# Performance work log

Hardware: AMD Instinct MI355X
Metric: run time of the kernel (lower is better)

Reference implementation:

```python
import jax, jax.numpy as jnp
import numpy as np

EPS = 1e-6
DROP_RATE = 0.25

def setup_inputs() -> dict:
    key = jax.random.key(0)
    k1, k2, k3 = jax.random.split(key, 3)
    B, S, D = 4, 2048, 2048
    inputs = jax.random.normal(k1, (B, S, D), dtype=jnp.float32)
    # keras 'uniform' initializer: U(-0.05, 0.05)
    W_1 = jax.random.uniform(k2, (D, D), dtype=jnp.float32, minval=-0.05, maxval=0.05)
    W_2 = jax.random.uniform(k3, (D, D), dtype=jnp.float32, minval=-0.05, maxval=0.05)
    return {"inputs": inputs, "W_1": W_1, "W_2": W_2}

def reference(inputs, W_1, W_2):
    # LayerNorm over last axis (no affine: gamma/beta unused in original call)
    mean = jnp.mean(inputs, axis=-1, keepdims=True)
    var = jnp.mean(jnp.square(inputs - mean), axis=-1, keepdims=True)
    x_norm = (inputs - mean) / jnp.sqrt(var + EPS)          # [B,S,D]
    # 2-layer MLP with relu
    h = jax.nn.relu(jnp.einsum('bsd,de->bse', x_norm, W_1))  # [B,S,D]
    y = jnp.einsum('bsd,de->bse', h, W_2)                    # [B,S,D]
    # dropout(0.25), inverted scaling, fixed key for determinism
    keep = jax.random.bernoulli(jax.random.key(1), 1.0 - DROP_RATE, y.shape)
    y_drop = jnp.where(keep, y / (1.0 - DROP_RATE), 0.0)
    return x_norm + y_drop
```

## Files before the change

kernel.cpp:

```cpp
#include <hip/hip_runtime.h>
#include <hip/hip_bf16.h>
#include <stdint.h>

#define M_DIM 8192
#define N_DIM 2048
#define K_DIM 2048

typedef __bf16 bf16x8_t __attribute__((ext_vector_type(8)));
typedef float f32x4_t __attribute__((ext_vector_type(4)));
typedef float f32x16_t __attribute__((ext_vector_type(16)));

__device__ __forceinline__ unsigned tf_rotl(unsigned x, int r) {
  return (x << r) | (x >> (32 - r));
}
__device__ __forceinline__ unsigned threefry_mask_bits(unsigned ctr) {
  unsigned x0 = 0u, x1 = ctr;
  const unsigned ks0 = 0u, ks1 = 1u, ks2 = 0x1BD11BDBu;
  x0 += ks0; x1 += ks1;
#define TFR(r) { x0 += x1; x1 = tf_rotl(x1, (r)); x1 ^= x0; }
  TFR(13) TFR(15) TFR(26) TFR(6)
  x0 += ks1; x1 += ks2 + 1u;
  TFR(17) TFR(29) TFR(16) TFR(24)
  x0 += ks2; x1 += ks0 + 2u;
  TFR(13) TFR(15) TFR(26) TFR(6)
  x0 += ks0; x1 += ks1 + 3u;
  TFR(17) TFR(29) TFR(16) TFR(24)
  x0 += ks1; x1 += ks2 + 4u;
  TFR(13) TFR(15) TFR(26) TFR(6)
  x0 += ks2; x1 += ks0 + 5u;
#undef TFR
  return x0 ^ x1;
}

__device__ __forceinline__ void gload_lds16(const __hip_bfloat16* g, unsigned short* l) {
  __builtin_amdgcn_global_load_lds(
      (const __attribute__((address_space(1))) unsigned int*)g,
      (__attribute__((address_space(3))) unsigned int*)l,
      16, 0, 0);
}

__global__ __launch_bounds__(256) void prep_kernel(
    const float* __restrict__ X,  __hip_bfloat16* __restrict__ Xn,
    const float* __restrict__ W1, const float* __restrict__ W2,
    __hip_bfloat16* __restrict__ W1t, __hip_bfloat16* __restrict__ W2t) {
  const int bid = blockIdx.x;
  if (bid < M_DIM) {
    const int row = bid;
    const float4* xv = (const float4*)(X + (size_t)row * K_DIM);
    float4 v0 = xv[threadIdx.x];
    float4 v1 = xv[threadIdx.x + 256];
    float s  = v0.x + v0.y + v0.z + v0.w + v1.x + v1.y + v1.z + v1.w;
    float ss = v0.x*v0.x + v0.y*v0.y + v0.z*v0.z + v0.w*v0.w
             + v1.x*v1.x + v1.y*v1.y + v1.z*v1.z + v1.w*v1.w;
#pragma unroll
    for (int off = 32; off > 0; off >>= 1) {
      s  += __shfl_xor(s, off);
      ss += __shfl_xor(ss, off);
    }
    __shared__ float rs[4], rss[4];
    const int wave = threadIdx.x >> 6;
    if ((threadIdx.x & 63) == 0) { rs[wave] = s; rss[wave] = ss; }
    __syncthreads();
    float S  = rs[0] + rs[1] + rs[2] + rs[3];
    float SS = rss[0] + rss[1] + rss[2] + rss[3];
    float mean = S * (1.0f / 2048.0f);
    float var  = SS * (1.0f / 2048.0f) - mean * mean;
    float rstd = 1.0f / sqrtf(var + 1e-6f);
    float vv[8] = {v0.x, v0.y, v0.z, v0.w, v1.x, v1.y, v1.z, v1.w};
    unsigned short o[8];
#pragma unroll
    for (int i = 0; i < 8; i++) {
      __hip_bfloat16 b = __float2bfloat16((vv[i] - mean) * rstd);
      o[i] = *(unsigned short*)&b;
    }
    ushort4* dst = (ushort4*)(Xn + (size_t)row * K_DIM);
    dst[threadIdx.x]       = make_ushort4(o[0], o[1], o[2], o[3]);
    dst[threadIdx.x + 256] = make_ushort4(o[4], o[5], o[6], o[7]);
  } else {
    const int t = bid - M_DIM;
    const int z  = t >> 12;
    const int r  = t & 4095;
    const int bx = r & 63;
    const int by = r >> 6;
    const int tx = threadIdx.x & 31;
    const int ty = threadIdx.x >> 5;
    __shared__ float tile[32][33];
    const float* src = z ? W2 : W1;
    __hip_bfloat16* dst = z ? W2t : W1t;
    int x = bx * 32 + tx;
    int y = by * 32 + ty;
#pragma unroll
    for (int i = 0; i < 32; i += 8)
      tile[ty + i][tx] = src[(size_t)(y + i) * N_DIM + x];
    __syncthreads();
    int xo = by * 32 + tx;
    int yo = bx * 32 + ty;
#pragma unroll
    for (int i = 0; i < 32; i += 8)
      dst[(size_t)(yo + i) * K_DIM + xo] = __float2bfloat16(tile[tx][ty + i]);
  }
}

template <int EPI>
__global__ __launch_bounds__(256) void gemm128(
    const __hip_bfloat16* __restrict__ A,
    const __hip_bfloat16* __restrict__ Bt,
    const __hip_bfloat16* __restrict__ Xn,
    __hip_bfloat16* __restrict__ Hout,
    float* __restrict__ Fout) {
  __shared__ unsigned short As[2][128 * 64];
  __shared__ unsigned short Bs[2][128 * 64];
  const int tid  = threadIdx.x;
  const int lane = tid & 63;
  const int wave = tid >> 6;
  const int wm = wave >> 1, wn = wave & 1;
  const int mBase = blockIdx.x * 128;
  const int nBase = blockIdx.y * 128;

  f32x16_t acc[2][2];
#pragma unroll
  for (int i = 0; i < 2; i++)
#pragma unroll
    for (int j = 0; j < 2; j++)
#pragma unroll
      for (int e = 0; e < 16; e++) acc[i][j][e] = 0.0f;

  const int rowIn  = lane >> 3;
  const int csrc   = ((lane & 7) ^ (rowIn & 7)) << 3;
  const __hip_bfloat16* aSrc[4];
  const __hip_bfloat16* bSrc[4];
  int sDst[4];
#pragma unroll
  for (int j = 0; j < 4; j++) {
    const int ca = wave + 4 * j;
    aSrc[j] = A  + (size_t)(mBase + 8 * ca + rowIn) * K_DIM + csrc;
    bSrc[j] = Bt + (size_t)(nBase + 8 * ca + rowIn) * K_DIM + csrc;
    sDst[j] = ca * 512;
  }

  const int r32 = lane & 31;
  const int kg  = lane >> 5;
  const int sw  = r32 & 7;
  const int rowA0 = (wm * 64 +      r32) * 64;
  const int rowA1 = (wm * 64 + 32 + r32) * 64;
  const int rowB0 = (wn * 64 +      r32) * 64;
  const int rowB1 = (wn * 64 + 32 + r32) * 64;

#define STAGE(buf, k0)                                        \
  {                                                           \
    _Pragma("unroll")                                         \
    for (int j = 0; j < 4; j++) {                             \
      gload_lds16(aSrc[j] + (k0), &As[buf][sDst[j]]);         \
      gload_lds16(bSrc[j] + (k0), &Bs[buf][sDst[j]]);         \
    }                                                         \
  }

#define COMPUTE(buf)                                                            \
  {                                                                             \
    _Pragma("unroll")                                                           \
    for (int ks = 0; ks < 4; ks++) {                                            \
      const int ck = (((ks << 1) | kg) ^ sw) << 3;                              \
      bf16x8_t a0 = *(const bf16x8_t*)(&As[buf][rowA0 + ck]);                   \
      bf16x8_t a1 = *(const bf16x8_t*)(&As[buf][rowA1 + ck]);                   \
      bf16x8_t b0 = *(const bf16x8_t*)(&Bs[buf][rowB0 + ck]);                   \
      bf16x8_t b1 = *(const bf16x8_t*)(&Bs[buf][rowB1 + ck]);                   \
      acc[0][0] = __builtin_amdgcn_mfma_f32_32x32x16_bf16(a0, b0, acc[0][0], 0, 0, 0); \
      acc[0][1] = __builtin_amdgcn_mfma_f32_32x32x16_bf16(a0, b1, acc[0][1], 0, 0, 0); \
      acc[1][0] = __builtin_amdgcn_mfma_f32_32x32x16_bf16(a1, b0, acc[1][0], 0, 0, 0); \
      acc[1][1] = __builtin_amdgcn_mfma_f32_32x32x16_bf16(a1, b1, acc[1][1], 0, 0, 0); \
    }                                                                           \
  }

#define BAR() __builtin_amdgcn_s_barrier()
#define VMW(n)  asm volatile("s_waitcnt vmcnt(" #n ")" ::: "memory")

#define TSTEP(BUF, STG, KNEXT, VMODE)                                    \
  {                                                                      \
    COMPUTE(BUF)                                                         \
    BAR();                               \
    if (STG) { STAGE(BUF, KNEXT) }                                       \
    if ((VMODE) == 0) { VMW(8); } else if ((VMODE) == 1) { VMW(0); }     \
    if ((VMODE) != 2) { BAR(); }              \
  }

  STAGE(0, 0)
  STAGE(1, 64)
  VMW(8);
  BAR();

  for (int k0 = 0; k0 < 1920; k0 += 128) {
    TSTEP(0, 1, k0 + 128, 0)
    TSTEP(1, 1, k0 + 192, 0)
  }
  TSTEP(0, 0, 0, 1)
  TSTEP(1, 0, 0, 2)

#undef TSTEP
#undef STAGE
#undef COMPUTE
#undef BAR
#undef VMW

  const int mRow = mBase + wm * 64;
  const int nCol = nBase + wn * 64;
#pragma unroll
  for (int mt = 0; mt < 2; mt++) {
#pragma unroll
    for (int nt = 0; nt < 2; nt++) {
      const int col = nCol + nt * 32 + r32;
#pragma unroll
      for (int r = 0; r < 16; r++) {
        const int row = mRow + mt * 32 + (r & 3) + ((r >> 2) << 3) + (kg << 2);
        float v = acc[mt][nt][r];
        size_t j = (size_t)row * N_DIM + col;
        if (EPI == 0) {
          Hout[j] = __float2bfloat16(fmaxf(v, 0.0f));
        } else {
          unsigned bits = threefry_mask_bits((unsigned)j);
          float y  = (bits < 0xC0000000u) ? v * (1.0f / 0.75f) : 0.0f;
          Fout[j]  = __bfloat162float(Xn[j]) + y;
        }
      }
    }
  }
}

extern "C" void kernel_launch(void* const* d_in, const int* in_sizes, int n_in,
                              void* d_out, int out_size, void* d_ws, size_t ws_size,
                              hipStream_t stream) {
  (void)in_sizes; (void)n_in; (void)out_size; (void)ws_size;
  const float* X  = (const float*)d_in[0];
  const float* W1 = (const float*)d_in[1];
  const float* W2 = (const float*)d_in[2];
  float* out = (float*)d_out;

  unsigned char* ws = (unsigned char*)d_ws;
  __hip_bfloat16* Xn  = (__hip_bfloat16*)(ws);
  __hip_bfloat16* H   = (__hip_bfloat16*)(ws + ((size_t)32 << 20));
  __hip_bfloat16* W1t = (__hip_bfloat16*)(ws + ((size_t)64 << 20));
  __hip_bfloat16* W2t = (__hip_bfloat16*)(ws + ((size_t)72 << 20));

  prep_kernel<<<dim3(2 * M_DIM, 1, 1), 256, 0, stream>>>(X, Xn, W1, W2, W1t, W2t);
  gemm128<0><<<dim3(M_DIM / 128, N_DIM / 128), 256, 0, stream>>>(Xn, W1t, nullptr, H, nullptr);
  gemm128<1><<<dim3(M_DIM / 128, N_DIM / 128), 256, 0, stream>>>(H, W2t, Xn, nullptr, out);
}
```

Baseline: 317.9 us.

## Use eight waves per 128x128 GEMM tile with 64x32 per-wave subtiles

Doubles the block to 512 threads so each of eight waves computes a 64x32 subtile with two MFMA accumulators instead of four. Staging loads are split across twice as many waves and the vmcnt waits are adjusted to match. The aim is more waves per CU to hide LDS and global latency and fewer registers per wave. In exchange each wave does less MFMA work per LDS fragment read, so LDS traffic per FLOP goes up.

```diff
diff --git a/kernel.cpp b/kernel.cpp
--- a/kernel.cpp
+++ b/kernel.cpp
@@ -102,7 +102,7 @@
 }
 
 template <int EPI>
-__global__ __launch_bounds__(256) void gemm128(
+__global__ __launch_bounds__(512, 4) void gemm128(
     const __hip_bfloat16* __restrict__ A,
     const __hip_bfloat16* __restrict__ Bt,
     const __hip_bfloat16* __restrict__ Xn,
@@ -113,26 +113,23 @@
   const int tid  = threadIdx.x;
   const int lane = tid & 63;
   const int wave = tid >> 6;
-  const int wm = wave >> 1, wn = wave & 1;
+  const int wm = wave >> 2;
+  const int wn = wave & 3;
   const int mBase = blockIdx.x * 128;
   const int nBase = blockIdx.y * 128;
 
-  f32x16_t acc[2][2];
-#pragma unroll
-  for (int i = 0; i < 2; i++)
-#pragma unroll
-    for (int j = 0; j < 2; j++)
-#pragma unroll
-      for (int e = 0; e < 16; e++) acc[i][j][e] = 0.0f;
+  f32x16_t acc0, acc1;
+#pragma unroll
+  for (int e = 0; e < 16; e++) { acc0[e] = 0.0f; acc1[e] = 0.0f; }
 
   const int rowIn  = lane >> 3;
   const int csrc   = ((lane & 7) ^ (rowIn & 7)) << 3;
-  const __hip_bfloat16* aSrc[4];
-  const __hip_bfloat16* bSrc[4];
-  int sDst[4];
-#pragma unroll
-  for (int j = 0; j < 4; j++) {
-    const int ca = wave + 4 * j;
+  const __hip_bfloat16* aSrc[2];
+  const __hip_bfloat16* bSrc[2];
+  int sDst[2];
+#pragma unroll
+  for (int j = 0; j < 2; j++) {
+    const int ca = wave + 8 * j;
     aSrc[j] = A  + (size_t)(mBase + 8 * ca + rowIn) * K_DIM + csrc;
     bSrc[j] = Bt + (size_t)(nBase + 8 * ca + rowIn) * K_DIM + csrc;
     sDst[j] = ca * 512;
@@ -141,15 +138,13 @@
   const int r32 = lane & 31;
   const int kg  = lane >> 5;
   const int sw  = r32 & 7;
-  const int rowA0 = (wm * 64 +      r32) * 64;
-  const int rowA1 = (wm * 64 + 32 + r32) * 64;
-  const int rowB0 = (wn * 64 +      r32) * 64;
-  const int rowB1 = (wn * 64 + 32 + r32) * 64;
+  const int rowA = (wm * 64 + r32) * 64;
+  const int rowB = (wn * 32 + r32) * 64;
 
 #define STAGE(buf, k0)                                        \
   {                                                           \
     _Pragma("unroll")                                         \
-    for (int j = 0; j < 4; j++) {                             \
+    for (int j = 0; j < 2; j++) {                             \
       gload_lds16(aSrc[j] + (k0), &As[buf][sDst[j]]);         \
       gload_lds16(bSrc[j] + (k0), &Bs[buf][sDst[j]]);         \
     }                                                         \
@@ -160,14 +155,11 @@
     _Pragma("unroll")                                                           \
     for (int ks = 0; ks < 4; ks++) {                                            \
       const int ck = (((ks << 1) | kg) ^ sw) << 3;                              \
-      bf16x8_t a0 = *(const bf16x8_t*)(&As[buf][rowA0 + ck]);                   \
-      bf16x8_t a1 = *(const bf16x8_t*)(&As[buf][rowA1 + ck]);                   \
-      bf16x8_t b0 = *(const bf16x8_t*)(&Bs[buf][rowB0 + ck]);                   \
-      bf16x8_t b1 = *(const bf16x8_t*)(&Bs[buf][rowB1 + ck]);                   \
-      acc[0][0] = __builtin_amdgcn_mfma_f32_32x32x16_bf16(a0, b0, acc[0][0], 0, 0, 0); \
-      acc[0][1] = __builtin_amdgcn_mfma_f32_32x32x16_bf16(a0, b1, acc[0][1], 0, 0, 0); \
-      acc[1][0] = __builtin_amdgcn_mfma_f32_32x32x16_bf16(a1, b0, acc[1][0], 0, 0, 0); \
-      acc[1][1] = __builtin_amdgcn_mfma_f32_32x32x16_bf16(a1, b1, acc[1][1], 0, 0, 0); \
+      bf16x8_t a0 = *(const bf16x8_t*)(&As[buf][rowA + ck]);                    \
+      bf16x8_t a1 = *(const bf16x8_t*)(&As[buf][rowA + 2048 + ck]);             \
+      bf16x8_t b  = *(const bf16x8_t*)(&Bs[buf][rowB + ck]);                    \
+      acc0 = __builtin_amdgcn_mfma_f32_32x32x16_bf16(a0, b, acc0, 0, 0, 0);     \
+      acc1 = __builtin_amdgcn_mfma_f32_32x32x16_bf16(a1, b, acc1, 0, 0, 0);     \
     }                                                                           \
   }
 
@@ -179,13 +171,13 @@
     COMPUTE(BUF)                                                         \
     BAR();                               \
     if (STG) { STAGE(BUF, KNEXT) }                                       \
-    if ((VMODE) == 0) { VMW(8); } else if ((VMODE) == 1) { VMW(0); }     \
+    if ((VMODE) == 0) { VMW(4); } else if ((VMODE) == 1) { VMW(0); }     \
     if ((VMODE) != 2) { BAR(); }              \
   }
 
   STAGE(0, 0)
   STAGE(1, 64)
-  VMW(8);
+  VMW(4);
   BAR();
 
   for (int k0 = 0; k0 < 1920; k0 += 128) {
@@ -201,25 +193,21 @@
 #undef BAR
 #undef VMW
 
+  const int col = nBase + wn * 32 + r32;
   const int mRow = mBase + wm * 64;
-  const int nCol = nBase + wn * 64;
 #pragma unroll
   for (int mt = 0; mt < 2; mt++) {
 #pragma unroll
-    for (int nt = 0; nt < 2; nt++) {
-      const int col = nCol + nt * 32 + r32;
-#pragma unroll
-      for (int r = 0; r < 16; r++) {
-        const int row = mRow + mt * 32 + (r & 3) + ((r >> 2) << 3) + (kg << 2);
-        float v = acc[mt][nt][r];
-        size_t j = (size_t)row * N_DIM + col;
-        if (EPI == 0) {
-          Hout[j] = __float2bfloat16(fmaxf(v, 0.0f));
-        } else {
-          unsigned bits = threefry_mask_bits((unsigned)j);
-          float y  = (bits < 0xC0000000u) ? v * (1.0f / 0.75f) : 0.0f;
-          Fout[j]  = __bfloat162float(Xn[j]) + y;
-        }
+    for (int r = 0; r < 16; r++) {
+      const int row = mRow + mt * 32 + (r & 3) + ((r >> 2) << 3) + (kg << 2);
+      float v = mt ? acc1[r] : acc0[r];
+      size_t j = (size_t)row * N_DIM + col;
+      if (EPI == 0) {
+        Hout[j] = __float2bfloat16(fmaxf(v, 0.0f));
+      } else {
+        unsigned bits = threefry_mask_bits((unsigned)j);
+        float y  = (bits < 0xC0000000u) ? v * (1.0f / 0.75f) : 0.0f;
+        Fout[j]  = __bfloat162float(Xn[j]) + y;
       }
     }
   }
@@ -241,6 +229,6 @@
   __hip_bfloat16* W2t = (__hip_bfloat16*)(ws + ((size_t)72 << 20));
 
   prep_kernel<<<dim3(2 * M_DIM, 1, 1), 256, 0, stream>>>(X, Xn, W1, W2, W1t, W2t);
-  gemm128<0><<<dim3(M_DIM / 128, N_DIM / 128), 256, 0, stream>>>(Xn, W1t, nullptr, H, nullptr);
-  gemm128<1><<<dim3(M_DIM / 128, N_DIM / 128), 256, 0, stream>>>(H, W2t, Xn, nullptr, out);
-}
+  gemm128<0><<<dim3(M_DIM / 128, N_DIM / 128), dim3(512, 1, 1), 0, stream>>>(Xn, W1t, nullptr, H, nullptr);
+  gemm128<1><<<dim3(M_DIM / 128, N_DIM / 128), dim3(512, 1, 1), 0, stream>>>(H, W2t, Xn, nullptr, out);
+}
```

After: 318.2 us. No clear change (+0.1%).
